# Kernel tuning notes

Hardware: AMD Instinct MI355X
Metric: run time of the kernel (lower is better)

## Reference

```python
import jax, jax.numpy as jnp
import numpy as np

D = 768
H = 12
HD = D // H
EPS = 1e-8  # torch cosine_similarity default eps


def setup_inputs() -> dict:
    key = jax.random.key(0)
    ks = jax.random.split(key, 16)
    bs, T, K = 8, 2048, 512
    s = 0.02
    return {
        "hidden_states": jax.random.normal(ks[0], (bs, T, D), jnp.float32),
        "attention_mask": jnp.ones((bs, T), jnp.int32),
        "pooled_hidden_states": jax.random.normal(ks[1], (bs, D), jnp.float32),
        "kg_key": jax.random.normal(ks[2], (bs, K, D), jnp.float32),
        "kg_value": jax.random.normal(ks[3], (bs, K, D), jnp.float32),
        "beta": jnp.ones((H,), jnp.float32),
        "Wq": jax.random.normal(ks[4], (D, D), jnp.float32) * s,
        "bq": jnp.zeros((D,), jnp.float32),
        "Wk": jax.random.normal(ks[5], (D, D), jnp.float32) * s,
        "bk": jnp.zeros((D,), jnp.float32),
        "Wv": jax.random.normal(ks[6], (D, D), jnp.float32) * s,
        "bv": jnp.zeros((D,), jnp.float32),
        "Wo": jax.random.normal(ks[7], (D, D), jnp.float32) * s,
        "bo": jnp.zeros((D,), jnp.float32),
    }


def reference(hidden_states, attention_mask, pooled_hidden_states, kg_key, kg_value,
              beta, Wq, bq, Wk, bk, Wv, bv, Wo, bo):
    bs, T, _ = hidden_states.shape
    K = kg_key.shape[1]
    # cosine similarity between pooled state and each KG key: [bs, K]
    pn = pooled_hidden_states / jnp.maximum(
        jnp.linalg.norm(pooled_hidden_states, axis=-1, keepdims=True), EPS)
    kn = kg_key / jnp.maximum(jnp.linalg.norm(kg_key, axis=-1, keepdims=True), EPS)
    sim = jnp.einsum("bd,bkd->bk", pn, kn)

    scale = HD ** -0.5
    # projections (torch Linear: y = x @ W.T + b)
    q = ((hidden_states @ Wq.T + bq) * scale).reshape(bs, T, H, HD).transpose(0, 2, 1, 3)
    k = (kg_value @ Wk.T + bk).reshape(bs, K, H, HD).transpose(0, 2, 1, 3)
    v = (kg_value @ Wv.T + bv).reshape(bs, K, H, HD).transpose(0, 2, 1, 3)

    # scores + per-head cosine-sim bias: [bs, H, T, K]
    scores = jnp.einsum("bhtd,bhkd->bhtk", q, k)
    scores = scores + beta[None, :, None, None] * sim[:, None, None, :]
    probs = jax.nn.softmax(scores, axis=-1)

    out = jnp.einsum("bhtk,bhkd->bhtd", probs, v)
    out = out.transpose(0, 2, 1, 3).reshape(bs, T, D)
    return out @ Wo.T + bo
```

## Files before the change

kernel.cpp:

```cpp
#include <hip/hip_runtime.h>
#include <math.h>

#define D_MODEL 768
#define NHEAD   12
#define HD      64
#define SEQ_T   2048
#define SEQ_K   512
#define BS      8
#define EPS_COS 1e-8f
#define LOG2E   1.44269504f

typedef short  bf16x8 __attribute__((ext_vector_type(8)));
typedef float  f32x4  __attribute__((ext_vector_type(4)));

__device__ __forceinline__ ushort f2bf(float x) {
    unsigned b = __float_as_uint(x);
    return (ushort)((b + 0x7FFF + ((b >> 16) & 1)) >> 16);
}
__device__ __forceinline__ unsigned cvt_pk_bf16(float lo, float hi) {
    unsigned r;
    asm("v_cvt_pk_bf16_f32 %0, %1, %2" : "=v"(r) : "v"(lo), "v"(hi));
    return r;
}
__device__ __forceinline__ float exp2_fast(float x) {
    float r;
    asm("v_exp_f32 %0, %1" : "=v"(r) : "v"(x));
    return r;
}

__device__ __forceinline__ void async_copy16(void* lds_base, const void* g_src) {
    __builtin_amdgcn_global_load_lds(
        (const __attribute__((address_space(1))) unsigned int*)g_src,
        (__attribute__((address_space(3))) unsigned int*)lds_base,
        16, 0, 0);
}

__global__ __launch_bounds__(256) void cvt6_kernel(
    const float* __restrict__ hidden, const float* __restrict__ kgv,
    const float* __restrict__ Wq, const float* __restrict__ Wk,
    const float* __restrict__ Wv, const float* __restrict__ Wo,
    ushort* __restrict__ hb, ushort* __restrict__ gb,
    ushort* __restrict__ wqb, ushort* __restrict__ wkb,
    ushort* __restrict__ wvb, ushort* __restrict__ wob)
{
    const long total = 4521984;
    for (long i = (long)blockIdx.x * 256 + threadIdx.x; i < total;
         i += (long)gridDim.x * 256) {
        const float* s; ushort* d; long off;
        if (i < 3145728)      { s = hidden; d = hb;  off = i; }
        else if (i < 3932160) { s = kgv;    d = gb;  off = i - 3145728; }
        else if (i < 4079616) { s = Wq;     d = wqb; off = i - 3932160; }
        else if (i < 4227072) { s = Wk;     d = wkb; off = i - 4079616; }
        else if (i < 4374528) { s = Wv;     d = wvb; off = i - 4227072; }
        else                  { s = Wo;     d = wob; off = i - 4374528; }
        float4 v = reinterpret_cast<const float4*>(s)[off];
        ushort4 o;
        o.x = f2bf(v.x); o.y = f2bf(v.y); o.z = f2bf(v.z); o.w = f2bf(v.w);
        reinterpret_cast<ushort4*>(d)[off] = o;
    }
}

__global__ __launch_bounds__(256, 3) void fused_proj_sim_kernel(
    const ushort* __restrict__ hb, const ushort* __restrict__ gb,
    const ushort* __restrict__ Wqb, const float* __restrict__ bq,
    const ushort* __restrict__ Wkb, const float* __restrict__ bk_,
    const ushort* __restrict__ Wvb, const float* __restrict__ bv_,
    const float* __restrict__ pooled, const float* __restrict__ kg_key,
    const float* __restrict__ beta,
    ushort* __restrict__ qout, ushort* __restrict__ kout,
    ushort* __restrict__ vtout, float* __restrict__ bsim, float qscale)
{
    __shared__ __align__(16) char lds[32768];
    constexpr int Kd = D_MODEL;
    const int bid = blockIdx.x;
    const int tid = threadIdx.x, wid = tid >> 6, l = tid & 63;
    const int g = l >> 4, c = l & 15;

    if (bid < 1152) {
        ushort* As = (ushort*)lds;
        ushort* Bs = (ushort*)(lds + 16384);
        const bool isQ = bid < 768;
        int m0, n0c;
        const ushort* Asrc;
        const ushort* Wsel;
        if (isQ) {
            m0 = (bid & 127) * 128; n0c = (bid >> 7) * 128;
            Asrc = hb;
            Wsel = Wqb + (size_t)n0c * Kd;
        } else {
            int q = bid - 768;
            m0 = (q & 31) * 128; n0c = (q >> 5) * 128;
            Asrc = gb;
            Wsel = (n0c < 768) ? (Wkb + (size_t)n0c * Kd)
                               : (Wvb + (size_t)(n0c - 768) * Kd);
        }
        const int wm = (wid >> 1) * 64, wn = (wid & 1) * 64;

        f32x4 acc[4][4] = {};
        for (int k0 = 0; k0 < Kd; k0 += 64) {
            __syncthreads();
#pragma unroll
            for (int it = 0; it < 4; ++it) {
                int L = wid * 4096 + it * 1024 + l * 16;
                int row = L >> 7;
                int gbk = ((L >> 4) & 7) ^ (row & 7);
                async_copy16((char*)As + wid * 4096 + it * 1024,
                             Asrc + (size_t)(m0 + row) * Kd + k0 + gbk * 8);
            }
#pragma unroll
            for (int it = 0; it < 4; ++it) {
                int L = wid * 4096 + it * 1024 + l * 16;
                int row = L >> 7;
                int gbk = ((L >> 4) & 7) ^ (row & 7);
                async_copy16((char*)Bs + wid * 4096 + it * 1024,
                             Wsel + (size_t)row * Kd + k0 + gbk * 8);
            }
            __syncthreads();

            bf16x8 af[4][2], bf[4][2];
#pragma unroll
            for (int mt = 0; mt < 4; ++mt)
#pragma unroll
                for (int ks = 0; ks < 2; ++ks) {
                    int row = wm + mt * 16 + c;
                    af[mt][ks] = *(const bf16x8*)((const char*)As + row * 128 +
                                                  (((ks * 4 + g) ^ (row & 7)) << 4));
                }
#pragma unroll
            for (int nt = 0; nt < 4; ++nt)
#pragma unroll
                for (int ks = 0; ks < 2; ++ks) {
                    int row = wn + nt * 16 + c;
                    bf[nt][ks] = *(const bf16x8*)((const char*)Bs + row * 128 +
                                                  (((ks * 4 + g) ^ (row & 7)) << 4));
                }
            __builtin_amdgcn_s_setprio(1);
#pragma unroll
            for (int mt = 0; mt < 4; ++mt)
#pragma unroll
                for (int nt = 0; nt < 4; ++nt) {
                    acc[mt][nt] = __builtin_amdgcn_mfma_f32_16x16x32_bf16(
                        af[mt][0], bf[nt][0], acc[mt][nt], 0, 0, 0);
                    acc[mt][nt] = __builtin_amdgcn_mfma_f32_16x16x32_bf16(
                        af[mt][1], bf[nt][1], acc[mt][nt], 0, 0, 0);
                }
            __builtin_amdgcn_s_setprio(0);
        }

        if (isQ) {
#pragma unroll
            for (int mt = 0; mt < 4; ++mt)
#pragma unroll
                for (int nt = 0; nt < 4; ++nt) {
                    int col = n0c + wn + nt * 16 + c;
                    float bv = bq[col];
#pragma unroll
                    for (int j = 0; j < 4; ++j) {
                        int row = m0 + wm + mt * 16 + g * 4 + j;
                        qout[(size_t)row * Kd + col] =
                            f2bf((acc[mt][nt][j] + bv) * qscale);
                    }
                }
        } else if (n0c < 768) {
#pragma unroll
            for (int mt = 0; mt < 4; ++mt)
#pragma unroll
                for (int nt = 0; nt < 4; ++nt) {
                    int col = n0c + wn + nt * 16 + c;
                    float bbk = bk_[col];
#pragma unroll
                    for (int j = 0; j < 4; ++j) {
                        int row = m0 + wm + mt * 16 + g * 4 + j;
                        kout[(size_t)row * Kd + col] = f2bf(acc[mt][nt][j] + bbk);
                    }
                }
        } else {
            int b = m0 >> 9;
            int kc = (m0 >> 7) & 3;
#pragma unroll
            for (int mt = 0; mt < 4; ++mt) {
                int kb0 = wm + mt * 16 + 4 * g;
                int kp0 = ((kb0 >> 5) << 5) | (((kb0 >> 2) & 3) << 3) |
                          (((kb0 >> 4) & 1) << 2);
#pragma unroll
                for (int nt = 0; nt < 4; ++nt) {
                    int d_full = (n0c - 768) + wn + nt * 16 + c;
                    int h2 = d_full >> 6, dd = d_full & 63;
                    float bbv = bv_[d_full];
                    unsigned u0 = cvt_pk_bf16(acc[mt][nt][0] + bbv,
                                              acc[mt][nt][1] + bbv);
                    unsigned u1 = cvt_pk_bf16(acc[mt][nt][2] + bbv,
                                              acc[mt][nt][3] + bbv);
                    size_t base = ((size_t)(b * NHEAD + h2) * HD + dd) * SEQ_K
                                  + kc * 128 + kp0;
                    uint2 st2; st2.x = u0; st2.y = u1;
                    *(uint2*)(vtout + base) = st2;
                }
            }
        }
    } else {
        int wrow = (bid - 1152) * 4 + (tid >> 6);
        int lane = tid & 63;
        int b  = wrow >> 9;
        int kk = wrow & 511;
        const float* p   = pooled + (size_t)b * D_MODEL;
        const float* key = kg_key + ((size_t)b * SEQ_K + kk) * D_MODEL;
        float dpk = 0.f, dkk = 0.f, dpp = 0.f;
        for (int i = lane; i < D_MODEL; i += 64) {
            float pv = p[i], kv = key[i];
            dpk += pv * kv; dkk += kv * kv; dpp += pv * pv;
        }
        for (int off = 32; off; off >>= 1) {
            dpk += __shfl_xor(dpk, off);
            dkk += __shfl_xor(dkk, off);
            dpp += __shfl_xor(dpp, off);
        }
        if (lane == 0) {
            float np_ = fmaxf(sqrtf(dpp), EPS_COS);
            float nk_ = fmaxf(sqrtf(dkk), EPS_COS);
            float sv = (dpk / (np_ * nk_)) * LOG2E;
#pragma unroll
            for (int h = 0; h < NHEAD; ++h)
                bsim[(size_t)(b * NHEAD + h) * SEQ_K + kk] = beta[h] * sv;
        }
    }
}

__global__ __launch_bounds__(256, 2) void gemm_o_kernel(
    const ushort* __restrict__ A, const ushort* __restrict__ W,
    const float* __restrict__ bias, float* __restrict__ out_f32)
{
    constexpr int Kd = D_MODEL;
    __shared__ __align__(16) ushort As[128 * 64];
    __shared__ __align__(16) ushort Bs[128 * 64];
    const int tid = threadIdx.x, wid = tid >> 6, l = tid & 63;
    const int g = l >> 4, c = l & 15;
    const int m0 = blockIdx.x * 128, n0 = blockIdx.y * 128;
    const int wm = (wid >> 1) * 64, wn = (wid & 1) * 64;

    f32x4 acc[4][4] = {};

    for (int k0 = 0; k0 < Kd; k0 += 64) {
        __syncthreads();
#pragma unroll
        for (int it = 0; it < 4; ++it) {
            int L = wid * 4096 + it * 1024 + l * 16;
            int row = L >> 7;
            int gb = ((L >> 4) & 7) ^ (row & 7);
            async_copy16((char*)As + wid * 4096 + it * 1024,
                         A + (size_t)(m0 + row) * Kd + k0 + gb * 8);
        }
#pragma unroll
        for (int it = 0; it < 4; ++it) {
            int L = wid * 4096 + it * 1024 + l * 16;
            int row = L >> 7;
            int gb = ((L >> 4) & 7) ^ (row & 7);
            async_copy16((char*)Bs + wid * 4096 + it * 1024,
                         W + (size_t)(n0 + row) * Kd + k0 + gb * 8);
        }
        __syncthreads();

        bf16x8 af[4][2], bf[4][2];
#pragma unroll
        for (int mt = 0; mt < 4; ++mt)
#pragma unroll
            for (int ks = 0; ks < 2; ++ks) {
                int row = wm + mt * 16 + c;
                af[mt][ks] = *(const bf16x8*)((const char*)As + row * 128 +
                                              (((ks * 4 + g) ^ (row & 7)) << 4));
            }
#pragma unroll
        for (int nt = 0; nt < 4; ++nt)
#pragma unroll
            for (int ks = 0; ks < 2; ++ks) {
                int row = wn + nt * 16 + c;
                bf[nt][ks] = *(const bf16x8*)((const char*)Bs + row * 128 +
                                              (((ks * 4 + g) ^ (row & 7)) << 4));
            }
        __builtin_amdgcn_s_setprio(1);
#pragma unroll
        for (int mt = 0; mt < 4; ++mt)
#pragma unroll
            for (int nt = 0; nt < 4; ++nt) {
                acc[mt][nt] = __builtin_amdgcn_mfma_f32_16x16x32_bf16(
                    af[mt][0], bf[nt][0], acc[mt][nt], 0, 0, 0);
                acc[mt][nt] = __builtin_amdgcn_mfma_f32_16x16x32_bf16(
                    af[mt][1], bf[nt][1], acc[mt][nt], 0, 0, 0);
            }
        __builtin_amdgcn_s_setprio(0);
    }

#pragma unroll
    for (int mt = 0; mt < 4; ++mt)
#pragma unroll
        for (int nt = 0; nt < 4; ++nt) {
            int col = n0 + wn + nt * 16 + c;
            float bv = bias[col];
#pragma unroll
            for (int j = 0; j < 4; ++j) {
                int row = m0 + wm + mt * 16 + g * 4 + j;
                out_f32[(size_t)row * Kd + col] = acc[mt][nt][j] + bv;
            }
        }
}

__global__ __launch_bounds__(256, 4) void attn_mfma_kernel(
    const ushort* __restrict__ qb, const ushort* __restrict__ kbp,
    const ushort* __restrict__ vt, const float* __restrict__ bsim,
    ushort* __restrict__ ctx)
{
    int bid = blockIdx.x;
    int w = (bid & 7) * 192 + (bid >> 3);
    int tile = w & 15; int rest = w >> 4; int h = rest % 12; int b = rest / 12;
    int t0 = tile * 128;
    int tid = threadIdx.x, wid = tid >> 6, l = tid & 63;
    int g = l >> 4, c = l & 15;

    __shared__ __align__(16) char KV[2][16384];

    const ushort* srck[2]; const ushort* srcv[2];
    int offk[2], offv[2];
#pragma unroll
    for (int it = 0; it < 2; ++it) {
        int L = wid * 2048 + it * 1024 + l * 16;
        int row = L >> 7;
        int gb = ((L >> 4) & 7) ^ (row & 7);
        srck[it] = kbp + (size_t)(b * SEQ_K + row) * D_MODEL + h * HD + gb * 8;
        offk[it] = wid * 2048 + it * 1024;
        int d = row;
        int blk = (L >> 4) & 7;
        int gblk = blk ^ (d & 7);
        srcv[it] = vt + ((size_t)((b * NHEAD + h) * HD + d)) * SEQ_K + gblk * 8;
        offv[it] = 8192 + wid * 2048 + it * 1024;
    }

#pragma unroll
    for (int it = 0; it < 4; ++it) {
        int L = wid * 4096 + it * 1024 + l * 16;
        int row = L >> 7;
        int gb = ((L >> 4) & 7) ^ (row & 7);
        async_copy16(&KV[0][0] + wid * 4096 + it * 1024,
                     qb + (size_t)(b * SEQ_T + t0 + row) * D_MODEL + h * HD + gb * 8);
    }
    const float* bsrow = bsim + (size_t)(b * NHEAD + h) * SEQ_K;
    __syncthreads();

    bf16x8 aq[2][2];
#pragma unroll
    for (int sub = 0; sub < 2; ++sub)
#pragma unroll
        for (int ks = 0; ks < 2; ++ks) {
            int row = wid * 32 + sub * 16 + c;
            aq[sub][ks] = *(const bf16x8*)(&KV[0][0] + row * 128 +
                                           (((ks * 4 + g) ^ (row & 7)) << 4));
        }
    __syncthreads();

#pragma unroll
    for (int it = 0; it < 2; ++it) {
        async_copy16(&KV[0][0] + offk[it], srck[it]);
        async_copy16(&KV[0][0] + offv[it], srcv[it]);
    }

    const bf16x8 ones8 = {(short)0x3F80, (short)0x3F80, (short)0x3F80, (short)0x3F80,
                          (short)0x3F80, (short)0x3F80, (short)0x3F80, (short)0x3F80};
    f32x4 oacc[2][4] = {};
    f32x4 oSum[2] = {};
    int cur = 0;

    for (int kc = 0; kc < 8; ++kc) {
        __syncthreads();
        if (kc < 7) {
            int nxt = cur ^ 1;
#pragma unroll
            for (int it = 0; it < 2; ++it) {
                srck[it] += 64 * D_MODEL;
                async_copy16(&KV[nxt][0] + offk[it], srck[it]);
                srcv[it] += 64;
                async_copy16(&KV[nxt][0] + offv[it], srcv[it]);
            }
        }
        const char* Kb = &KV[cur][0];
        const char* Vb = &KV[cur][0] + 8192;

#pragma unroll
        for (int kb = 0; kb < 2; ++kb) {
            f32x4 st[2][2];
            __builtin_amdgcn_s_setprio(1);
#pragma unroll
            for (int n2 = 0; n2 < 2; ++n2) {
                int nt = 2 * kb + n2;
                f32x4 cinit = *(const f32x4*)(bsrow + kc * 64 + nt * 16 + 4 * g);
                int krow = nt * 16 + c;
                bf16x8 ak0 = *(const bf16x8*)(Kb + krow * 128 +
                                              ((g ^ (krow & 7)) << 4));
                bf16x8 ak1 = *(const bf16x8*)(Kb + krow * 128 +
                                              (((4 + g) ^ (krow & 7)) << 4));
#pragma unroll
                for (int sub = 0; sub < 2; ++sub) {
                    st[sub][n2] = __builtin_amdgcn_mfma_f32_16x16x32_bf16(
                        ak0, aq[sub][0], cinit, 0, 0, 0);
                    st[sub][n2] = __builtin_amdgcn_mfma_f32_16x16x32_bf16(
                        ak1, aq[sub][1], st[sub][n2], 0, 0, 0);
                }
            }
            __builtin_amdgcn_s_setprio(0);

            bf16x8 pa[2];
#pragma unroll
            for (int sub = 0; sub < 2; ++sub) {
                f32x4 e0, e1;
#pragma unroll
                for (int j = 0; j < 4; ++j) {
                    e0[j] = exp2_fast(st[sub][0][j]);
                    e1[j] = exp2_fast(st[sub][1][j]);
                }
                union { unsigned u[4]; bf16x8 v; } pk;
                pk.u[0] = cvt_pk_bf16(e0[0], e0[1]);
                pk.u[1] = cvt_pk_bf16(e0[2], e0[3]);
                pk.u[2] = cvt_pk_bf16(e1[0], e1[1]);
                pk.u[3] = cvt_pk_bf16(e1[2], e1[3]);
                pa[sub] = pk.v;
            }

            __builtin_amdgcn_s_setprio(1);
#pragma unroll
            for (int sub = 0; sub < 2; ++sub)
                oSum[sub] = __builtin_amdgcn_mfma_f32_16x16x32_bf16(
                    pa[sub], ones8, oSum[sub], 0, 0, 0);
#pragma unroll
            for (int dt = 0; dt < 4; ++dt) {
                int d = dt * 16 + c;
                int blk = kb * 4 + g;
                int sb = blk ^ (d & 7);
                bf16x8 bv = *(const bf16x8*)(Vb + d * 128 + (sb << 4));
#pragma unroll
                for (int sub = 0; sub < 2; ++sub)
                    oacc[sub][dt] = __builtin_amdgcn_mfma_f32_16x16x32_bf16(
                        pa[sub], bv, oacc[sub][dt], 0, 0, 0);
            }
            __builtin_amdgcn_s_setprio(0);
        }
        cur ^= 1;
    }

#pragma unroll
    for (int sub = 0; sub < 2; ++sub) {
        f32x4 invL;
#pragma unroll
        for (int j = 0; j < 4; ++j) invL[j] = 1.f / oSum[sub][j];
#pragma unroll
        for (int dt = 0; dt < 4; ++dt)
#pragma unroll
            for (int j = 0; j < 4; ++j) {
                int trow = t0 + wid * 32 + sub * 16 + 4 * g + j;
                int d = dt * 16 + c;
                ctx[(size_t)(b * SEQ_T + trow) * D_MODEL + h * HD + d] =
                    f2bf(oacc[sub][dt][j] * invL[j]);
            }
    }
}

extern "C" void kernel_launch(void* const* d_in, const int* in_sizes, int n_in,
                              void* d_out, int out_size, void* d_ws, size_t ws_size,
                              hipStream_t stream)
{
    const float* hidden  = (const float*)d_in[0];
    const float* pooled  = (const float*)d_in[2];
    const float* kg_key  = (const float*)d_in[3];
    const float* kg_val  = (const float*)d_in[4];
    const float* beta    = (const float*)d_in[5];
    const float* Wq = (const float*)d_in[6];  const float* bq = (const float*)d_in[7];
    const float* Wk = (const float*)d_in[8];  const float* bk = (const float*)d_in[9];
    const float* Wv = (const float*)d_in[10]; const float* bv = (const float*)d_in[11];
    const float* Wo = (const float*)d_in[12]; const float* bo = (const float*)d_in[13];
    float* out = (float*)d_out;

    const size_t MQ = (size_t)BS * SEQ_T;
    const size_t MK = (size_t)BS * SEQ_K;
    const size_t DW = D_MODEL * D_MODEL;

    float*  bsim = (float*)d_ws;
    ushort* wqb  = (ushort*)(bsim + BS * NHEAD * SEQ_K);
    ushort* wkb  = wqb + DW;
    ushort* wvb  = wkb + DW;
    ushort* wob  = wvb + DW;
    ushort* hb   = wob + DW;
    ushort* gb   = hb  + MQ * D_MODEL;
    ushort* qbb  = gb  + MK * D_MODEL;
    ushort* kbb  = qbb + MQ * D_MODEL;
    ushort* vtb  = kbb + MK * D_MODEL;
    ushort* ctxb = vtb + MK * D_MODEL;

    cvt6_kernel<<<2048, 256, 0, stream>>>(
        hidden, kg_val, Wq, Wk, Wv, Wo, hb, gb, wqb, wkb, wvb, wob);

    fused_proj_sim_kernel<<<2176, 256, 0, stream>>>(
        hb, gb, wqb, bq, wkb, bk, wvb, bv,
        pooled, kg_key, beta, qbb, kbb, vtb, bsim, 0.125f * LOG2E);

    attn_mfma_kernel<<<BS * NHEAD * (SEQ_T / 128), 256, 0, stream>>>(
        qbb, kbb, vtb, bsim, ctxb);

    gemm_o_kernel<<<dim3(MQ / 128, 6), 256, 0, stream>>>(ctxb, wob, bo, out);
}
```

Before: 118.2 us.

## Move cosine-sim into convert kernel, swizzle projection blocks, raise O-GEMM occupancy

The cosine-similarity bias computation moves out of the projection GEMM kernel and into the fp32-to-bf16 conversion kernel, which becomes a 2D grid with one y-slice per tensor plus one for the sim. The projection kernel now launches only the GEMM tiles, with a block-index swizzle (stride 144 across 8 groups) intended to improve L2 reuse and XCD distribution. The output-projection GEMM launch bound is raised from 2 to 3 waves per SIMD to allow more occupancy. This costs a less balanced conversion grid, since the y-slices have very different sizes, and some risk of register pressure in the O GEMM.

```diff
diff --git a/kernel.cpp b/kernel.cpp
--- a/kernel.cpp
+++ b/kernel.cpp
@@ -35,171 +35,20 @@
         16, 0, 0);
 }
 
-__global__ __launch_bounds__(256) void cvt6_kernel(
+__global__ __launch_bounds__(256) void cvt_sim_kernel(
     const float* __restrict__ hidden, const float* __restrict__ kgv,
     const float* __restrict__ Wq, const float* __restrict__ Wk,
     const float* __restrict__ Wv, const float* __restrict__ Wo,
     ushort* __restrict__ hb, ushort* __restrict__ gb,
     ushort* __restrict__ wqb, ushort* __restrict__ wkb,
-    ushort* __restrict__ wvb, ushort* __restrict__ wob)
+    ushort* __restrict__ wvb, ushort* __restrict__ wob,
+    const float* __restrict__ pooled, const float* __restrict__ kg_key,
+    const float* __restrict__ beta, float* __restrict__ bsim)
 {
-    const long total = 4521984;
-    for (long i = (long)blockIdx.x * 256 + threadIdx.x; i < total;
-         i += (long)gridDim.x * 256) {
-        const float* s; ushort* d; long off;
-        if (i < 3145728)      { s = hidden; d = hb;  off = i; }
-        else if (i < 3932160) { s = kgv;    d = gb;  off = i - 3145728; }
-        else if (i < 4079616) { s = Wq;     d = wqb; off = i - 3932160; }
-        else if (i < 4227072) { s = Wk;     d = wkb; off = i - 4079616; }
-        else if (i < 4374528) { s = Wv;     d = wvb; off = i - 4227072; }
-        else                  { s = Wo;     d = wob; off = i - 4374528; }
-        float4 v = reinterpret_cast<const float4*>(s)[off];
-        ushort4 o;
-        o.x = f2bf(v.x); o.y = f2bf(v.y); o.z = f2bf(v.z); o.w = f2bf(v.w);
-        reinterpret_cast<ushort4*>(d)[off] = o;
-    }
-}
-
-__global__ __launch_bounds__(256, 3) void fused_proj_sim_kernel(
-    const ushort* __restrict__ hb, const ushort* __restrict__ gb,
-    const ushort* __restrict__ Wqb, const float* __restrict__ bq,
-    const ushort* __restrict__ Wkb, const float* __restrict__ bk_,
-    const ushort* __restrict__ Wvb, const float* __restrict__ bv_,
-    const float* __restrict__ pooled, const float* __restrict__ kg_key,
-    const float* __restrict__ beta,
-    ushort* __restrict__ qout, ushort* __restrict__ kout,
-    ushort* __restrict__ vtout, float* __restrict__ bsim, float qscale)
-{
-    __shared__ __align__(16) char lds[32768];
-    constexpr int Kd = D_MODEL;
-    const int bid = blockIdx.x;
-    const int tid = threadIdx.x, wid = tid >> 6, l = tid & 63;
-    const int g = l >> 4, c = l & 15;
-
-    if (bid < 1152) {
-        ushort* As = (ushort*)lds;
-        ushort* Bs = (ushort*)(lds + 16384);
-        const bool isQ = bid < 768;
-        int m0, n0c;
-        const ushort* Asrc;
-        const ushort* Wsel;
-        if (isQ) {
-            m0 = (bid & 127) * 128; n0c = (bid >> 7) * 128;
-            Asrc = hb;
-            Wsel = Wqb + (size_t)n0c * Kd;
-        } else {
-            int q = bid - 768;
-            m0 = (q & 31) * 128; n0c = (q >> 5) * 128;
-            Asrc = gb;
-            Wsel = (n0c < 768) ? (Wkb + (size_t)n0c * Kd)
-                               : (Wvb + (size_t)(n0c - 768) * Kd);
-        }
-        const int wm = (wid >> 1) * 64, wn = (wid & 1) * 64;
-
-        f32x4 acc[4][4] = {};
-        for (int k0 = 0; k0 < Kd; k0 += 64) {
-            __syncthreads();
-#pragma unroll
-            for (int it = 0; it < 4; ++it) {
-                int L = wid * 4096 + it * 1024 + l * 16;
-                int row = L >> 7;
-                int gbk = ((L >> 4) & 7) ^ (row & 7);
-                async_copy16((char*)As + wid * 4096 + it * 1024,
-                             Asrc + (size_t)(m0 + row) * Kd + k0 + gbk * 8);
-            }
-#pragma unroll
-            for (int it = 0; it < 4; ++it) {
-                int L = wid * 4096 + it * 1024 + l * 16;
-                int row = L >> 7;
-                int gbk = ((L >> 4) & 7) ^ (row & 7);
-                async_copy16((char*)Bs + wid * 4096 + it * 1024,
-                             Wsel + (size_t)row * Kd + k0 + gbk * 8);
-            }
-            __syncthreads();
-
-            bf16x8 af[4][2], bf[4][2];
-#pragma unroll
-            for (int mt = 0; mt < 4; ++mt)
-#pragma unroll
-                for (int ks = 0; ks < 2; ++ks) {
-                    int row = wm + mt * 16 + c;
-                    af[mt][ks] = *(const bf16x8*)((const char*)As + row * 128 +
-                                                  (((ks * 4 + g) ^ (row & 7)) << 4));
-                }
-#pragma unroll
-            for (int nt = 0; nt < 4; ++nt)
-#pragma unroll
-                for (int ks = 0; ks < 2; ++ks) {
-                    int row = wn + nt * 16 + c;
-                    bf[nt][ks] = *(const bf16x8*)((const char*)Bs + row * 128 +
-                                                  (((ks * 4 + g) ^ (row & 7)) << 4));
-                }
-            __builtin_amdgcn_s_setprio(1);
-#pragma unroll
-            for (int mt = 0; mt < 4; ++mt)
-#pragma unroll
-                for (int nt = 0; nt < 4; ++nt) {
-                    acc[mt][nt] = __builtin_amdgcn_mfma_f32_16x16x32_bf16(
-                        af[mt][0], bf[nt][0], acc[mt][nt], 0, 0, 0);
-                    acc[mt][nt] = __builtin_amdgcn_mfma_f32_16x16x32_bf16(
-                        af[mt][1], bf[nt][1], acc[mt][nt], 0, 0, 0);
-                }
-            __builtin_amdgcn_s_setprio(0);
-        }
-
-        if (isQ) {
-#pragma unroll
-            for (int mt = 0; mt < 4; ++mt)
-#pragma unroll
-                for (int nt = 0; nt < 4; ++nt) {
-                    int col = n0c + wn + nt * 16 + c;
-                    float bv = bq[col];
-#pragma unroll
-                    for (int j = 0; j < 4; ++j) {
-                        int row = m0 + wm + mt * 16 + g * 4 + j;
-                        qout[(size_t)row * Kd + col] =
-                            f2bf((acc[mt][nt][j] + bv) * qscale);
-                    }
-                }
-        } else if (n0c < 768) {
-#pragma unroll
-            for (int mt = 0; mt < 4; ++mt)
-#pragma unroll
-                for (int nt = 0; nt < 4; ++nt) {
-                    int col = n0c + wn + nt * 16 + c;
-                    float bbk = bk_[col];
-#pragma unroll
-                    for (int j = 0; j < 4; ++j) {
-                        int row = m0 + wm + mt * 16 + g * 4 + j;
-                        kout[(size_t)row * Kd + col] = f2bf(acc[mt][nt][j] + bbk);
-                    }
-                }
-        } else {
-            int b = m0 >> 9;
-            int kc = (m0 >> 7) & 3;
-#pragma unroll
-            for (int mt = 0; mt < 4; ++mt) {
-                int kb0 = wm + mt * 16 + 4 * g;
-                int kp0 = ((kb0 >> 5) << 5) | (((kb0 >> 2) & 3) << 3) |
-                          (((kb0 >> 4) & 1) << 2);
-#pragma unroll
-                for (int nt = 0; nt < 4; ++nt) {
-                    int d_full = (n0c - 768) + wn + nt * 16 + c;
-                    int h2 = d_full >> 6, dd = d_full & 63;
-                    float bbv = bv_[d_full];
-                    unsigned u0 = cvt_pk_bf16(acc[mt][nt][0] + bbv,
-                                              acc[mt][nt][1] + bbv);
-                    unsigned u1 = cvt_pk_bf16(acc[mt][nt][2] + bbv,
-                                              acc[mt][nt][3] + bbv);
-                    size_t base = ((size_t)(b * NHEAD + h2) * HD + dd) * SEQ_K
-                                  + kc * 128 + kp0;
-                    uint2 st2; st2.x = u0; st2.y = u1;
-                    *(uint2*)(vtout + base) = st2;
-                }
-            }
-        }
-    } else {
-        int wrow = (bid - 1152) * 4 + (tid >> 6);
+    const int y = blockIdx.y;
+    const int tid = threadIdx.x;
+    if (y == 6) {
+        int wrow = blockIdx.x * 4 + (tid >> 6);
         int lane = tid & 63;
         int b  = wrow >> 9;
         int kk = wrow & 511;
@@ -223,10 +72,164 @@
             for (int h = 0; h < NHEAD; ++h)
                 bsim[(size_t)(b * NHEAD + h) * SEQ_K + kk] = beta[h] * sv;
         }
-    }
-}
-
-__global__ __launch_bounds__(256, 2) void gemm_o_kernel(
+        return;
+    }
+    const float* s; ushort* d; int n4;
+    switch (y) {
+        case 0:  s = hidden; d = hb;  n4 = 3145728; break;
+        case 1:  s = kgv;    d = gb;  n4 = 786432;  break;
+        case 2:  s = Wq;     d = wqb; n4 = 147456;  break;
+        case 3:  s = Wk;     d = wkb; n4 = 147456;  break;
+        case 4:  s = Wv;     d = wvb; n4 = 147456;  break;
+        default: s = Wo;     d = wob; n4 = 147456;  break;
+    }
+    for (int i = blockIdx.x * 256 + tid; i < n4; i += 1024 * 256) {
+        float4 v = reinterpret_cast<const float4*>(s)[i];
+        ushort4 o;
+        o.x = f2bf(v.x); o.y = f2bf(v.y); o.z = f2bf(v.z); o.w = f2bf(v.w);
+        reinterpret_cast<ushort4*>(d)[i] = o;
+    }
+}
+
+__global__ __launch_bounds__(256, 3) void fused_proj_kernel(
+    const ushort* __restrict__ hb, const ushort* __restrict__ gb,
+    const ushort* __restrict__ Wqb, const float* __restrict__ bq,
+    const ushort* __restrict__ Wkb, const float* __restrict__ bk_,
+    const ushort* __restrict__ Wvb, const float* __restrict__ bv_,
+    ushort* __restrict__ qout, ushort* __restrict__ kout,
+    ushort* __restrict__ vtout, float qscale)
+{
+    __shared__ __align__(16) char lds[32768];
+    constexpr int Kd = D_MODEL;
+    const int gidx = blockIdx.x;
+    const int sw = (gidx & 7) * 144 + (gidx >> 3);
+    const int tid = threadIdx.x, wid = tid >> 6, l = tid & 63;
+    const int g = l >> 4, c = l & 15;
+
+    ushort* As = (ushort*)lds;
+    ushort* Bs = (ushort*)(lds + 16384);
+    const bool isQ = sw < 768;
+    int m0, n0c;
+    const ushort* Asrc;
+    const ushort* Wsel;
+    if (isQ) {
+        m0 = (sw & 127) * 128; n0c = (sw >> 7) * 128;
+        Asrc = hb;
+        Wsel = Wqb + (size_t)n0c * Kd;
+    } else {
+        int q = sw - 768;
+        m0 = (q & 31) * 128; n0c = (q >> 5) * 128;
+        Asrc = gb;
+        Wsel = (n0c < 768) ? (Wkb + (size_t)n0c * Kd)
+                           : (Wvb + (size_t)(n0c - 768) * Kd);
+    }
+    const int wm = (wid >> 1) * 64, wn = (wid & 1) * 64;
+
+    f32x4 acc[4][4] = {};
+    for (int k0 = 0; k0 < Kd; k0 += 64) {
+        __syncthreads();
+#pragma unroll
+        for (int it = 0; it < 4; ++it) {
+            int L = wid * 4096 + it * 1024 + l * 16;
+            int row = L >> 7;
+            int gbk = ((L >> 4) & 7) ^ (row & 7);
+            async_copy16((char*)As + wid * 4096 + it * 1024,
+                         Asrc + (size_t)(m0 + row) * Kd + k0 + gbk * 8);
+        }
+#pragma unroll
+        for (int it = 0; it < 4; ++it) {
+            int L = wid * 4096 + it * 1024 + l * 16;
+            int row = L >> 7;
+            int gbk = ((L >> 4) & 7) ^ (row & 7);
+            async_copy16((char*)Bs + wid * 4096 + it * 1024,
+                         Wsel + (size_t)row * Kd + k0 + gbk * 8);
+        }
+        __syncthreads();
+
+        bf16x8 af[4][2], bf[4][2];
+#pragma unroll
+        for (int mt = 0; mt < 4; ++mt)
+#pragma unroll
+            for (int ks = 0; ks < 2; ++ks) {
+                int row = wm + mt * 16 + c;
+                af[mt][ks] = *(const bf16x8*)((const char*)As + row * 128 +
+                                              (((ks * 4 + g) ^ (row & 7)) << 4));
+            }
+#pragma unroll
+        for (int nt = 0; nt < 4; ++nt)
+#pragma unroll
+            for (int ks = 0; ks < 2; ++ks) {
+                int row = wn + nt * 16 + c;
+                bf[nt][ks] = *(const bf16x8*)((const char*)Bs + row * 128 +
+                                              (((ks * 4 + g) ^ (row & 7)) << 4));
+            }
+        __builtin_amdgcn_s_setprio(1);
+#pragma unroll
+        for (int mt = 0; mt < 4; ++mt)
+#pragma unroll
+            for (int nt = 0; nt < 4; ++nt) {
+                acc[mt][nt] = __builtin_amdgcn_mfma_f32_16x16x32_bf16(
+                    af[mt][0], bf[nt][0], acc[mt][nt], 0, 0, 0);
+                acc[mt][nt] = __builtin_amdgcn_mfma_f32_16x16x32_bf16(
+                    af[mt][1], bf[nt][1], acc[mt][nt], 0, 0, 0);
+            }
+        __builtin_amdgcn_s_setprio(0);
+    }
+
+    if (isQ) {
+#pragma unroll
+        for (int mt = 0; mt < 4; ++mt)
+#pragma unroll
+            for (int nt = 0; nt < 4; ++nt) {
+                int col = n0c + wn + nt * 16 + c;
+                float bv = bq[col];
+#pragma unroll
+                for (int j = 0; j < 4; ++j) {
+                    int row = m0 + wm + mt * 16 + g * 4 + j;
+                    qout[(size_t)row * Kd + col] =
+                        f2bf((acc[mt][nt][j] + bv) * qscale);
+                }
+            }
+    } else if (n0c < 768) {
+#pragma unroll
+        for (int mt = 0; mt < 4; ++mt)
+#pragma unroll
+            for (int nt = 0; nt < 4; ++nt) {
+                int col = n0c + wn + nt * 16 + c;
+                float bbk = bk_[col];
+#pragma unroll
+                for (int j = 0; j < 4; ++j) {
+                    int row = m0 + wm + mt * 16 + g * 4 + j;
+                    kout[(size_t)row * Kd + col] = f2bf(acc[mt][nt][j] + bbk);
+                }
+            }
+    } else {
+        int b = m0 >> 9;
+        int kc = (m0 >> 7) & 3;
+#pragma unroll
+        for (int mt = 0; mt < 4; ++mt) {
+            int kb0 = wm + mt * 16 + 4 * g;
+            int kp0 = ((kb0 >> 5) << 5) | (((kb0 >> 2) & 3) << 3) |
+                      (((kb0 >> 4) & 1) << 2);
+#pragma unroll
+            for (int nt = 0; nt < 4; ++nt) {
+                int d_full = (n0c - 768) + wn + nt * 16 + c;
+                int h2 = d_full >> 6, dd = d_full & 63;
+                float bbv = bv_[d_full];
+                unsigned u0 = cvt_pk_bf16(acc[mt][nt][0] + bbv,
+                                          acc[mt][nt][1] + bbv);
+                unsigned u1 = cvt_pk_bf16(acc[mt][nt][2] + bbv,
+                                          acc[mt][nt][3] + bbv);
+                size_t base = ((size_t)(b * NHEAD + h2) * HD + dd) * SEQ_K
+                              + kc * 128 + kp0;
+                uint2 st2; st2.x = u0; st2.y = u1;
+                *(uint2*)(vtout + base) = st2;
+            }
+        }
+    }
+}
+
+__global__ __launch_bounds__(256, 3) void gemm_o_kernel(
     const ushort* __restrict__ A, const ushort* __restrict__ W,
     const float* __restrict__ bias, float* __restrict__ out_f32)
 {
@@ -492,12 +495,12 @@
     ushort* vtb  = kbb + MK * D_MODEL;
     ushort* ctxb = vtb + MK * D_MODEL;
 
-    cvt6_kernel<<<2048, 256, 0, stream>>>(
-        hidden, kg_val, Wq, Wk, Wv, Wo, hb, gb, wqb, wkb, wvb, wob);
-
-    fused_proj_sim_kernel<<<2176, 256, 0, stream>>>(
-        hb, gb, wqb, bq, wkb, bk, wvb, bv,
-        pooled, kg_key, beta, qbb, kbb, vtb, bsim, 0.125f * LOG2E);
+    cvt_sim_kernel<<<dim3(1024, 7), 256, 0, stream>>>(
+        hidden, kg_val, Wq, Wk, Wv, Wo, hb, gb, wqb, wkb, wvb, wob,
+        pooled, kg_key, beta, bsim);
+
+    fused_proj_kernel<<<1152, 256, 0, stream>>>(
+        hb, gb, wqb, bq, wkb, bk, wvb, bv, qbb, kbb, vtb, 0.125f * LOG2E);
 
     attn_mfma_kernel<<<BS * NHEAD * (SEQ_T / 128), 256, 0, stream>>>(
         qbb, kbb, vtb, bsim, ctxb);
```

Measured after the change: 125.4 us. 6.1% more time.
